# Optimization experiments

Hardware: AMD Instinct MI355X
Metric: run time of the kernel (lower is better)

## Reference

```python
import jax, jax.numpy as jnp
import numpy as np

EPS = 1e-3  # tf.keras.layers.BatchNormalization default epsilon


def setup_inputs() -> dict:
    key = jax.random.key(0)
    k1, k2 = jax.random.split(key)
    B, N, F = 16, 8192, 256
    voxel_features = jax.random.normal(k1, (B, N, F), dtype=jnp.float32)
    num_valid_voxels = jax.random.randint(k2, (B,), 0, N, dtype=jnp.int32)
    gamma = jnp.ones((F,), dtype=jnp.float32)
    beta = jnp.zeros((F,), dtype=jnp.float32)
    return {
        "voxel_features": voxel_features,
        "num_valid_voxels": num_valid_voxels,
        "gamma": gamma,
        "beta": beta,
    }


def reference(voxel_features, num_valid_voxels, gamma, beta):
    # voxel_features: [B, N, F]; num_valid_voxels: [B]
    B, N, F = voxel_features.shape
    # mask[b, n] = n < num_valid_voxels[b]
    mask = (jnp.arange(N, dtype=jnp.int32)[None, :] < num_valid_voxels[:, None])
    maskf = mask.astype(voxel_features.dtype)[:, :, None]  # [B, N, 1]
    count = jnp.maximum(jnp.sum(num_valid_voxels).astype(voxel_features.dtype), 1.0)
    xm = voxel_features * maskf
    # Batch statistics over valid voxels only (per-feature), biased variance as BN uses
    mean = jnp.sum(xm, axis=(0, 1)) / count                      # [F]
    var = jnp.sum((voxel_features - mean) ** 2 * maskf, axis=(0, 1)) / count  # [F]
    inv_std = jax.lax.rsqrt(var + EPS)
    normed = (voxel_features - mean) * inv_std * gamma + beta
    # Padding positions are zeroed (the original pads unpadded outputs with zeros)
    return normed * maskf
```

## Files before the change

kernel.cpp:

```cpp
#include <hip/hip_runtime.h>

#define Bdim 16
#define Ndim 8192
#define Fdim 256
#define EPS 1e-3f

#define RED_BLOCKS_PER_BATCH 64
#define RED_BLOCKS (Bdim * RED_BLOCKS_PER_BATCH)
#define RED_ROWS_PER_BLOCK (Ndim / RED_BLOCKS_PER_BATCH)

#define NORM_BLOCKS 8192
#define TOTAL_CHUNKS (Bdim * Ndim * (Fdim / 4))

typedef float fx4 __attribute__((ext_vector_type(4)));


__global__ __launch_bounds__(512) void init_kernel(float* __restrict__ ws) {
    ws[threadIdx.x] = 0.0f;
}

__global__ __launch_bounds__(256) void reduce_kernel(
    const float* __restrict__ x, const int* __restrict__ nv,
    float* __restrict__ ws)
{
    __shared__ float lds_s[4][Fdim];
    __shared__ float lds_q[4][Fdim];
    const int tid = threadIdx.x;
    const int b   = blockIdx.x >> 6;
    const int rb0 = (blockIdx.x & 63) * RED_ROWS_PER_BLOCK;
    const int nvb = nv[b];
    int valid = nvb - rb0;
    valid = valid < 0 ? 0 : (valid > RED_ROWS_PER_BLOCK ? RED_ROWS_PER_BLOCK : valid);

    const int c = tid & 63;
    const int r = tid >> 6;
    const fx4* xb = (const fx4*)(x + ((size_t)b * Ndim + rb0) * Fdim) + c;

    float s0=0.f,s1=0.f,s2=0.f,s3=0.f, q0=0.f,q1=0.f,q2=0.f,q3=0.f;

    int i = r;
    for (; i + 12 < valid; i += 16) {
        const fx4 v0 = xb[(size_t)(i     ) * 64];
        const fx4 v1 = xb[(size_t)(i +  4) * 64];
        const fx4 v2 = xb[(size_t)(i +  8) * 64];
        const fx4 v3 = xb[(size_t)(i + 12) * 64];
        s0 += v0.x; q0 += v0.x*v0.x;  s1 += v0.y; q1 += v0.y*v0.y;
        s2 += v0.z; q2 += v0.z*v0.z;  s3 += v0.w; q3 += v0.w*v0.w;
        s0 += v1.x; q0 += v1.x*v1.x;  s1 += v1.y; q1 += v1.y*v1.y;
        s2 += v1.z; q2 += v1.z*v1.z;  s3 += v1.w; q3 += v1.w*v1.w;
        s0 += v2.x; q0 += v2.x*v2.x;  s1 += v2.y; q1 += v2.y*v2.y;
        s2 += v2.z; q2 += v2.z*v2.z;  s3 += v2.w; q3 += v2.w*v2.w;
        s0 += v3.x; q0 += v3.x*v3.x;  s1 += v3.y; q1 += v3.y*v3.y;
        s2 += v3.z; q2 += v3.z*v3.z;  s3 += v3.w; q3 += v3.w*v3.w;
    }
    for (; i < valid; i += 4) {
        const fx4 v = xb[(size_t)i * 64];
        s0 += v.x; q0 += v.x*v.x;  s1 += v.y; q1 += v.y*v.y;
        s2 += v.z; q2 += v.z*v.z;  s3 += v.w; q3 += v.w*v.w;
    }

    const int f0 = c * 4;
    lds_s[r][f0+0]=s0; lds_s[r][f0+1]=s1; lds_s[r][f0+2]=s2; lds_s[r][f0+3]=s3;
    lds_q[r][f0+0]=q0; lds_q[r][f0+1]=q1; lds_q[r][f0+2]=q2; lds_q[r][f0+3]=q3;
    __syncthreads();

    float ts = 0.0f, tq = 0.0f;
    #pragma unroll
    for (int rr = 0; rr < 4; rr++) { ts += lds_s[rr][tid]; tq += lds_q[rr][tid]; }
    unsafeAtomicAdd(&ws[tid], ts);
    unsafeAtomicAdd(&ws[Fdim + tid], tq);
}

__global__ __launch_bounds__(256) void norm_kernel(
    const float* __restrict__ x, const int* __restrict__ nv,
    const float* __restrict__ gamma, const float* __restrict__ beta,
    const float* __restrict__ ws, float* __restrict__ out)
{
    __shared__ float s_sc[Fdim], s_bi[Fdim];
    __shared__ int s_nv[Bdim];
    const int tid = threadIdx.x;
    if (tid < Bdim) s_nv[tid] = nv[tid];
    __syncthreads();
    {
        int cnt = 0;
        #pragma unroll
        for (int i = 0; i < Bdim; i++) cnt += s_nv[i];
        const float inv_count = 1.0f / fmaxf((float)cnt, 1.0f);
        const float mean = ws[tid] * inv_count;
        float var = fmaf(ws[Fdim + tid], inv_count, -mean * mean);
        var = fmaxf(var, 0.0f);
        const float s = rsqrtf(var + EPS) * gamma[tid];
        s_sc[tid] = s;
        s_bi[tid] = fmaf(-mean, s, beta[tid]);
    }
    __syncthreads();

    const int c = tid & 63;
    const fx4 sc = ((const fx4*)s_sc)[c];
    const fx4 bi = ((const fx4*)s_bi)[c];

    const int base = blockIdx.x * 256 + tid;
    const int stride = NORM_BLOCKS * 256;
    #pragma unroll
    for (int it = 0; it < TOTAL_CHUNKS / (NORM_BLOCKS * 256); it++) {
        const int idx = base + it * stride;
        const int row = idx >> 6;
        const int b = row >> 13;
        const int n = row & (Ndim - 1);
        fx4* po = (fx4*)out + idx;
        if (n < s_nv[b]) {
            const fx4 v = ((const fx4*)x)[idx];
            fx4 o;
            o.x = fmaf(v.x, sc.x, bi.x);
            o.y = fmaf(v.y, sc.y, bi.y);
            o.z = fmaf(v.z, sc.z, bi.z);
            o.w = fmaf(v.w, sc.w, bi.w);
            __builtin_nontemporal_store(o, po);
        } else {
            const fx4 z = {0.f, 0.f, 0.f, 0.f};
            __builtin_nontemporal_store(z, po);
        }
    }
}

extern "C" void kernel_launch(void* const* d_in, const int* in_sizes, int n_in,
                              void* d_out, int out_size, void* d_ws, size_t ws_size,
                              hipStream_t stream) {
    const float* x     = (const float*)d_in[0];
    const int*   nv    = (const int*)d_in[1];
    const float* gamma = (const float*)d_in[2];
    const float* beta  = (const float*)d_in[3];
    float* out = (float*)d_out;
    float* ws  = (float*)d_ws;

    init_kernel<<<1, 512, 0, stream>>>(ws);
    reduce_kernel<<<RED_BLOCKS, 256, 0, stream>>>(x, nv, ws);
    norm_kernel<<<NORM_BLOCKS, 256, 0, stream>>>(x, nv, gamma, beta, ws, out);
}
```

Baseline: 234.2 us.

## Interleave reduce rows across blocks and write padding zeros in reduce kernel

```diff
diff --git a/kernel.cpp b/kernel.cpp
--- a/kernel.cpp
+++ b/kernel.cpp
@@ -7,7 +7,8 @@
 
 #define RED_BLOCKS_PER_BATCH 64
 #define RED_BLOCKS (Bdim * RED_BLOCKS_PER_BATCH)
-#define RED_ROWS_PER_BLOCK (Ndim / RED_BLOCKS_PER_BATCH)
+#define RED_SLOTS 128
+#define SLOT_STRIDE_FX4 4096
 
 #define NORM_BLOCKS 8192
 #define TOTAL_CHUNKS (Bdim * Ndim * (Fdim / 4))
@@ -21,29 +22,30 @@
 
 __global__ __launch_bounds__(256) void reduce_kernel(
     const float* __restrict__ x, const int* __restrict__ nv,
-    float* __restrict__ ws)
+    float* __restrict__ ws, float* __restrict__ out)
 {
     __shared__ float lds_s[4][Fdim];
     __shared__ float lds_q[4][Fdim];
     const int tid = threadIdx.x;
     const int b   = blockIdx.x >> 6;
-    const int rb0 = (blockIdx.x & 63) * RED_ROWS_PER_BLOCK;
+    const int rbi = blockIdx.x & 63;
     const int nvb = nv[b];
-    int valid = nvb - rb0;
-    valid = valid < 0 ? 0 : (valid > RED_ROWS_PER_BLOCK ? RED_ROWS_PER_BLOCK : valid);
+    int kvalid = (nvb - rbi + 63) >> 6;
+    kvalid = kvalid < 0 ? 0 : (kvalid > RED_SLOTS ? RED_SLOTS : kvalid);
 
     const int c = tid & 63;
     const int r = tid >> 6;
-    const fx4* xb = (const fx4*)(x + ((size_t)b * Ndim + rb0) * Fdim) + c;
+    const fx4* xb = (const fx4*)(x   + ((size_t)b * Ndim + rbi) * Fdim) + c;
+    fx4*       ob = (fx4*)      (out + ((size_t)b * Ndim + rbi) * Fdim) + c;
 
     float s0=0.f,s1=0.f,s2=0.f,s3=0.f, q0=0.f,q1=0.f,q2=0.f,q3=0.f;
 
-    int i = r;
-    for (; i + 12 < valid; i += 16) {
-        const fx4 v0 = xb[(size_t)(i     ) * 64];
-        const fx4 v1 = xb[(size_t)(i +  4) * 64];
-        const fx4 v2 = xb[(size_t)(i +  8) * 64];
-        const fx4 v3 = xb[(size_t)(i + 12) * 64];
+    int k = r;
+    for (; k + 12 < kvalid; k += 16) {
+        const fx4 v0 = xb[(size_t)(k     ) * SLOT_STRIDE_FX4];
+        const fx4 v1 = xb[(size_t)(k +  4) * SLOT_STRIDE_FX4];
+        const fx4 v2 = xb[(size_t)(k +  8) * SLOT_STRIDE_FX4];
+        const fx4 v3 = xb[(size_t)(k + 12) * SLOT_STRIDE_FX4];
         s0 += v0.x; q0 += v0.x*v0.x;  s1 += v0.y; q1 += v0.y*v0.y;
         s2 += v0.z; q2 += v0.z*v0.z;  s3 += v0.w; q3 += v0.w*v0.w;
         s0 += v1.x; q0 += v1.x*v1.x;  s1 += v1.y; q1 += v1.y*v1.y;
@@ -53,10 +55,22 @@
         s0 += v3.x; q0 += v3.x*v3.x;  s1 += v3.y; q1 += v3.y*v3.y;
         s2 += v3.z; q2 += v3.z*v3.z;  s3 += v3.w; q3 += v3.w*v3.w;
     }
-    for (; i < valid; i += 4) {
-        const fx4 v = xb[(size_t)i * 64];
+    for (; k < kvalid; k += 4) {
+        const fx4 v = xb[(size_t)k * SLOT_STRIDE_FX4];
         s0 += v.x; q0 += v.x*v.x;  s1 += v.y; q1 += v.y*v.y;
         s2 += v.z; q2 += v.z*v.z;  s3 += v.w; q3 += v.w*v.w;
+    }
+    {
+        const fx4 z = {0.f, 0.f, 0.f, 0.f};
+        int kz = k;
+        for (; kz + 12 < RED_SLOTS; kz += 16) {
+            __builtin_nontemporal_store(z, ob + (size_t)(kz     ) * SLOT_STRIDE_FX4);
+            __builtin_nontemporal_store(z, ob + (size_t)(kz +  4) * SLOT_STRIDE_FX4);
+            __builtin_nontemporal_store(z, ob + (size_t)(kz +  8) * SLOT_STRIDE_FX4);
+            __builtin_nontemporal_store(z, ob + (size_t)(kz + 12) * SLOT_STRIDE_FX4);
+        }
+        for (; kz < RED_SLOTS; kz += 4)
+            __builtin_nontemporal_store(z, ob + (size_t)kz * SLOT_STRIDE_FX4);
     }
 
     const int f0 = c * 4;
@@ -107,7 +121,6 @@
         const int row = idx >> 6;
         const int b = row >> 13;
         const int n = row & (Ndim - 1);
-        fx4* po = (fx4*)out + idx;
         if (n < s_nv[b]) {
             const fx4 v = ((const fx4*)x)[idx];
             fx4 o;
@@ -115,10 +128,7 @@
             o.y = fmaf(v.y, sc.y, bi.y);
             o.z = fmaf(v.z, sc.z, bi.z);
             o.w = fmaf(v.w, sc.w, bi.w);
-            __builtin_nontemporal_store(o, po);
-        } else {
-            const fx4 z = {0.f, 0.f, 0.f, 0.f};
-            __builtin_nontemporal_store(z, po);
+            __builtin_nontemporal_store(o, (fx4*)out + idx);
         }
     }
 }
@@ -134,6 +144,6 @@
     float* ws  = (float*)d_ws;
 
     init_kernel<<<1, 512, 0, stream>>>(ws);
-    reduce_kernel<<<RED_BLOCKS, 256, 0, stream>>>(x, nv, ws);
+    reduce_kernel<<<RED_BLOCKS, 256, 0, stream>>>(x, nv, ws, out);
     norm_kernel<<<NORM_BLOCKS, 256, 0, stream>>>(x, nv, gamma, beta, ws, out);
 }
```

Result: slower. 240.1 us (+2.5%).

## Interleave reduction rows across blocks and pad atomic accumulator slots

Applied to the files above, without the earlier changes.

```diff
diff --git a/kernel.cpp b/kernel.cpp
--- a/kernel.cpp
+++ b/kernel.cpp
@@ -5,18 +5,22 @@
 #define Fdim 256
 #define EPS 1e-3f
 
-#define RED_BLOCKS_PER_BATCH 64
-#define RED_BLOCKS (Bdim * RED_BLOCKS_PER_BATCH)
-#define RED_ROWS_PER_BLOCK (Ndim / RED_BLOCKS_PER_BATCH)
+#define RB_PER_BATCH 64
+#define RED_BLOCKS (Bdim * RB_PER_BATCH)
+#define CHUNKS 16
+#define CHUNK_STRIDE_ROWS 512
+
+#define WS_PAD 68
+#define WS_VALS 512
+#define WS_FLOATS (WS_VALS * WS_PAD)
 
 #define NORM_BLOCKS 8192
-#define TOTAL_CHUNKS (Bdim * Ndim * (Fdim / 4))
+#define TOTAL_CHUNKS4 (Bdim * Ndim * (Fdim / 4))
 
 typedef float fx4 __attribute__((ext_vector_type(4)));
 
-
-__global__ __launch_bounds__(512) void init_kernel(float* __restrict__ ws) {
-    ws[threadIdx.x] = 0.0f;
+__global__ __launch_bounds__(256) void init_kernel(float* __restrict__ ws) {
+    ws[blockIdx.x * 256 + threadIdx.x] = 0.0f;
 }
 
 __global__ __launch_bounds__(256) void reduce_kernel(
@@ -27,23 +31,27 @@
     __shared__ float lds_q[4][Fdim];
     const int tid = threadIdx.x;
     const int b   = blockIdx.x >> 6;
-    const int rb0 = (blockIdx.x & 63) * RED_ROWS_PER_BLOCK;
+    const int rbi = blockIdx.x & 63;
     const int nvb = nv[b];
-    int valid = nvb - rb0;
-    valid = valid < 0 ? 0 : (valid > RED_ROWS_PER_BLOCK ? RED_ROWS_PER_BLOCK : valid);
 
     const int c = tid & 63;
     const int r = tid >> 6;
-    const fx4* xb = (const fx4*)(x + ((size_t)b * Ndim + rb0) * Fdim) + c;
+    const fx4* xb = (const fx4*)(x + (size_t)b * Ndim * Fdim) + c;
+
+    const int row_base = rbi * 8;
+    int t = nvb - row_base - 8;
+    int kfull = t < 0 ? 0 : (t >> 9) + 1;
+    if (kfull > CHUNKS) kfull = CHUNKS;
 
     float s0=0.f,s1=0.f,s2=0.f,s3=0.f, q0=0.f,q1=0.f,q2=0.f,q3=0.f;
 
-    int i = r;
-    for (; i + 12 < valid; i += 16) {
-        const fx4 v0 = xb[(size_t)(i     ) * 64];
-        const fx4 v1 = xb[(size_t)(i +  4) * 64];
-        const fx4 v2 = xb[(size_t)(i +  8) * 64];
-        const fx4 v3 = xb[(size_t)(i + 12) * 64];
+    int k = 0;
+    for (; k + 1 < kfull; k += 2) {
+        const size_t r0 = (size_t)(row_base + k * CHUNK_STRIDE_ROWS);
+        const fx4 v0 = xb[(r0 + r      ) * 64];
+        const fx4 v1 = xb[(r0 + r + 4  ) * 64];
+        const fx4 v2 = xb[(r0 + r + 512) * 64];
+        const fx4 v3 = xb[(r0 + r + 516) * 64];
         s0 += v0.x; q0 += v0.x*v0.x;  s1 += v0.y; q1 += v0.y*v0.y;
         s2 += v0.z; q2 += v0.z*v0.z;  s3 += v0.w; q3 += v0.w*v0.w;
         s0 += v1.x; q0 += v1.x*v1.x;  s1 += v1.y; q1 += v1.y*v1.y;
@@ -53,10 +61,28 @@
         s0 += v3.x; q0 += v3.x*v3.x;  s1 += v3.y; q1 += v3.y*v3.y;
         s2 += v3.z; q2 += v3.z*v3.z;  s3 += v3.w; q3 += v3.w*v3.w;
     }
-    for (; i < valid; i += 4) {
-        const fx4 v = xb[(size_t)i * 64];
-        s0 += v.x; q0 += v.x*v.x;  s1 += v.y; q1 += v.y*v.y;
-        s2 += v.z; q2 += v.z*v.z;  s3 += v.w; q3 += v.w*v.w;
+    for (; k < kfull; k++) {
+        const size_t r0 = (size_t)(row_base + k * CHUNK_STRIDE_ROWS);
+        const fx4 v0 = xb[(r0 + r    ) * 64];
+        const fx4 v1 = xb[(r0 + r + 4) * 64];
+        s0 += v0.x; q0 += v0.x*v0.x;  s1 += v0.y; q1 += v0.y*v0.y;
+        s2 += v0.z; q2 += v0.z*v0.z;  s3 += v0.w; q3 += v0.w*v0.w;
+        s0 += v1.x; q0 += v1.x*v1.x;  s1 += v1.y; q1 += v1.y*v1.y;
+        s2 += v1.z; q2 += v1.z*v1.z;  s3 += v1.w; q3 += v1.w*v1.w;
+    }
+    if (kfull < CHUNKS) {
+        const int row0 = row_base + kfull * CHUNK_STRIDE_ROWS;
+        const int n0 = row0 + r, n1 = row0 + r + 4;
+        if (n0 < nvb) {
+            const fx4 v = xb[(size_t)n0 * 64];
+            s0 += v.x; q0 += v.x*v.x;  s1 += v.y; q1 += v.y*v.y;
+            s2 += v.z; q2 += v.z*v.z;  s3 += v.w; q3 += v.w*v.w;
+        }
+        if (n1 < nvb) {
+            const fx4 v = xb[(size_t)n1 * 64];
+            s0 += v.x; q0 += v.x*v.x;  s1 += v.y; q1 += v.y*v.y;
+            s2 += v.z; q2 += v.z*v.z;  s3 += v.w; q3 += v.w*v.w;
+        }
     }
 
     const int f0 = c * 4;
@@ -67,8 +93,8 @@
     float ts = 0.0f, tq = 0.0f;
     #pragma unroll
     for (int rr = 0; rr < 4; rr++) { ts += lds_s[rr][tid]; tq += lds_q[rr][tid]; }
-    unsafeAtomicAdd(&ws[tid], ts);
-    unsafeAtomicAdd(&ws[Fdim + tid], tq);
+    unsafeAtomicAdd(&ws[tid * WS_PAD], ts);
+    unsafeAtomicAdd(&ws[(Fdim + tid) * WS_PAD], tq);
 }
 
 __global__ __launch_bounds__(256) void norm_kernel(
@@ -86,8 +112,8 @@
         #pragma unroll
         for (int i = 0; i < Bdim; i++) cnt += s_nv[i];
         const float inv_count = 1.0f / fmaxf((float)cnt, 1.0f);
-        const float mean = ws[tid] * inv_count;
-        float var = fmaf(ws[Fdim + tid], inv_count, -mean * mean);
+        const float mean = ws[tid * WS_PAD] * inv_count;
+        float var = fmaf(ws[(Fdim + tid) * WS_PAD], inv_count, -mean * mean);
         var = fmaxf(var, 0.0f);
         const float s = rsqrtf(var + EPS) * gamma[tid];
         s_sc[tid] = s;
@@ -102,7 +128,7 @@
     const int base = blockIdx.x * 256 + tid;
     const int stride = NORM_BLOCKS * 256;
     #pragma unroll
-    for (int it = 0; it < TOTAL_CHUNKS / (NORM_BLOCKS * 256); it++) {
+    for (int it = 0; it < TOTAL_CHUNKS4 / (NORM_BLOCKS * 256); it++) {
         const int idx = base + it * stride;
         const int row = idx >> 6;
         const int b = row >> 13;
@@ -133,7 +159,7 @@
     float* out = (float*)d_out;
     float* ws  = (float*)d_ws;
 
-    init_kernel<<<1, 512, 0, stream>>>(ws);
+    init_kernel<<<WS_FLOATS / 256, 256, 0, stream>>>(ws);
     reduce_kernel<<<RED_BLOCKS, 256, 0, stream>>>(x, nv, ws);
     norm_kernel<<<NORM_BLOCKS, 256, 0, stream>>>(x, nv, gamma, beta, ws, out);
 }
```

New measurement: 243.2 us. 3.9% more time.
